# Optimization experiments

Hardware: AMD Instinct MI355X
Metric: run time of the kernel (lower is better)

## Reference

```python
import jax, jax.numpy as jnp
import numpy as np

B, S, D_IN, D_OUT = 8, 2048, 4096, 4096
RANK, N_ADAPTERS = 16, 8


def setup_inputs() -> dict:
    key = jax.random.key(0)
    k = jax.random.split(key, 6)
    x = jax.random.normal(k[0], (B, S, D_IN), dtype=jnp.float32)
    W = jax.random.normal(k[1], (D_OUT, D_IN), dtype=jnp.float32) * 0.02
    bias = jax.random.normal(k[2], (D_OUT,), dtype=jnp.float32) * 0.02
    lora_a = jax.random.normal(k[3], (N_ADAPTERS, RANK, D_IN), dtype=jnp.float32) * 0.02
    lora_b = jax.random.normal(k[4], (N_ADAPTERS, D_OUT, RANK), dtype=jnp.float32) * 0.02
    adapter_indices = jax.random.randint(k[5], (B,), 0, N_ADAPTERS, dtype=jnp.int64)
    return {"x": x, "W": W, "bias": bias, "lora_a": lora_a,
            "lora_b": lora_b, "adapter_indices": adapter_indices}


def reference(x, W, bias, lora_a, lora_b, adapter_indices):
    # Base linear: y = x @ W.T + bias
    base = jnp.einsum('bsi,oi->bso', x, W) + bias
    # Per-batch-element adapter gather (adapter index is shared across the seq dim)
    a = lora_a[adapter_indices]            # [B, r, D_in]
    b = lora_b[adapter_indices]            # [B, D_out, r]
    inter = jnp.einsum('bsi,bri->bsr', x, a)      # x_group @ a_i.T
    lora_out = jnp.einsum('bsr,bor->bso', inter, b)  # intermediate @ b_i.T
    return base + lora_out
```

## Files before the change

### kernel.cpp

```cpp
#include <hip/hip_runtime.h>


#define S_DIM   2048
#define DIN     4096
#define DOUT    4096
#define RANK    16
#define M_DIM   16384
#define K_DIM   DIN
#define N_DIM   DOUT

typedef __attribute__((ext_vector_type(8))) short  short8;
typedef __attribute__((ext_vector_type(4))) float  floatx4;

__device__ __forceinline__ unsigned short f2bf(float f) {
  union { float f; unsigned int u; } v; v.f = f;
  return (unsigned short)((v.u + 0x7FFFu + ((v.u >> 16) & 1u)) >> 16);
}
__device__ __forceinline__ unsigned int pk2(float a, float b) {
  return (unsigned int)f2bf(a) | ((unsigned int)f2bf(b) << 16);
}

__device__ __forceinline__ int load_adapter(const int* __restrict__ p, int b) {
  bool i64 = (p[1] == 0) & (p[3] == 0) & (p[5] == 0) & (p[7] == 0);
  return i64 ? p[2 * b] : p[b];
}

__device__ __forceinline__ void async16(const unsigned short* g, unsigned short* s) {
  __builtin_amdgcn_global_load_lds(
      (const __attribute__((address_space(1))) void*)g,
      (__attribute__((address_space(3))) void*)s, 16, 0, 0);
}

__device__ __forceinline__ void pack16_pad(const float* __restrict__ src,
                                           unsigned short* dst) {
  float4 v0 = ((const float4*)src)[0], v1 = ((const float4*)src)[1],
         v2 = ((const float4*)src)[2], v3 = ((const float4*)src)[3];
  uint4 p0, p1;
  p0.x = pk2(v0.x, v0.y); p0.y = pk2(v0.z, v0.w);
  p0.z = pk2(v1.x, v1.y); p0.w = pk2(v1.z, v1.w);
  p1.x = pk2(v2.x, v2.y); p1.y = pk2(v2.z, v2.w);
  p1.z = pk2(v3.x, v3.y); p1.w = pk2(v3.z, v3.w);
  ((uint4*)dst)[0] = p0;
  ((uint4*)dst)[1] = p1;
  uint4 z = make_uint4(0u, 0u, 0u, 0u);
  ((uint4*)dst)[2] = z;
  ((uint4*)dst)[3] = z;
}

__global__ __launch_bounds__(256) void conv_w(const float* __restrict__ w,
                                              unsigned short* __restrict__ wbf) {
  size_t base = ((size_t)blockIdx.x * 256 + threadIdx.x) * 8;
  const float4* src = (const float4*)(w + base);
  float4 f0 = src[0], f1 = src[1];
  uint4 p;
  p.x = pk2(f0.x, f0.y); p.y = pk2(f0.z, f0.w);
  p.z = pk2(f1.x, f1.y); p.w = pk2(f1.z, f1.w);
  *(uint4*)(wbf + base) = p;
}

__global__ __launch_bounds__(256) void inter_conv_x(
    const float* __restrict__ x,
    const float* __restrict__ lora_a,
    const int* __restrict__ adapters,
    unsigned short* __restrict__ xbf,
    float* __restrict__ inter) {
  __shared__ floatx4 red[4][64];
  const int tid = threadIdx.x, wave = tid >> 6, lane = tid & 63;
  const int fr = lane & 15, fq = lane >> 4;
  const int row0 = blockIdx.x * 16;
  const int adapter = load_adapter(adapters, row0 >> 11);

  const float* xp = x + (size_t)(row0 + fr) * DIN;
  unsigned short* xq = xbf + (size_t)(row0 + fr) * DIN;
  const float* ap = lora_a + ((size_t)adapter * RANK + fr) * DIN;

  floatx4 acc = {};
  const int kbeg = wave * 1024, kend = kbeg + 1024;
  for (int k0 = kbeg; k0 < kend; k0 += 32) {
    const int k = k0 + fq * 8;
    float4 a0 = *(const float4*)(xp + k);
    float4 a1 = *(const float4*)(xp + k + 4);
    uint4 apk;
    apk.x = pk2(a0.x, a0.y); apk.y = pk2(a0.z, a0.w);
    apk.z = pk2(a1.x, a1.y); apk.w = pk2(a1.z, a1.w);
    *(uint4*)(xq + k) = apk;
    float4 b0 = *(const float4*)(ap + k);
    float4 b1 = *(const float4*)(ap + k + 4);
    uint4 bpk;
    bpk.x = pk2(b0.x, b0.y); bpk.y = pk2(b0.z, b0.w);
    bpk.z = pk2(b1.x, b1.y); bpk.w = pk2(b1.z, b1.w);
    short8 af = *(short8*)&apk;
    short8 bf_ = *(short8*)&bpk;
    acc = __builtin_amdgcn_mfma_f32_16x16x32_bf16(af, bf_, acc, 0, 0, 0);
  }
  red[wave][lane] = acc;
  __syncthreads();
  if (wave == 0) {
    floatx4 s = red[0][lane] + red[1][lane] + red[2][lane] + red[3][lane];
#pragma unroll
    for (int j = 0; j < 4; ++j)
      inter[(size_t)(row0 + fq * 4 + j) * RANK + fr] = s[j];
  }
}

__global__ __launch_bounds__(256, 2) void gemm_lora(
    const unsigned short* __restrict__ A,
    const unsigned short* __restrict__ Bw,
    const float* __restrict__ bias,
    const float* __restrict__ inter,
    const float* __restrict__ lora_b,
    const int* __restrict__ adapters,
    float* __restrict__ out) {
  __shared__ unsigned short As[128 * 32];
  __shared__ unsigned short Bs[128 * 32];
  const int tid = threadIdx.x;
  const int wave = tid >> 6, lane = tid & 63;
  const int wm = wave >> 1, wn = wave & 1;
  const int row0 = blockIdx.y * 128, col0 = blockIdx.x * 128;

  const int lrow = lane >> 2, lcol = (lane & 3) * 8;
  const unsigned short* ag = A  + (size_t)(row0 + wave * 32 + lrow) * K_DIM + lcol;
  const unsigned short* bg = Bw + (size_t)(col0 + wave * 32 + lrow) * K_DIM + lcol;
  unsigned short* asd = As + wave * 1024;
  unsigned short* bsd = Bs + wave * 1024;

  const int fr = lane & 15, fq = lane >> 4;
  const unsigned short* afp = As + ((wm * 64 + fr) * 32 + fq * 8);
  const unsigned short* bfp = Bs + ((wn * 64 + fr) * 32 + fq * 8);

  floatx4 acc[4][4] = {};

  for (int k0 = 0; k0 < K_DIM; k0 += 32) {
    __syncthreads();
    async16(ag + k0, asd);
    async16(ag + k0 + (size_t)16 * K_DIM, asd + 512);
    async16(bg + k0, bsd);
    async16(bg + k0 + (size_t)16 * K_DIM, bsd + 512);
    __syncthreads();
    short8 af[4], bf[4];
#pragma unroll
    for (int i = 0; i < 4; ++i) af[i] = *(const short8*)(afp + i * 512);
#pragma unroll
    for (int i = 0; i < 4; ++i) bf[i] = *(const short8*)(bfp + i * 512);
#pragma unroll
    for (int mt = 0; mt < 4; ++mt)
#pragma unroll
      for (int nt = 0; nt < 4; ++nt)
        acc[mt][nt] = __builtin_amdgcn_mfma_f32_16x16x32_bf16(
            af[mt], bf[nt], acc[mt][nt], 0, 0, 0);
  }

  const int adapter = load_adapter(adapters, row0 >> 11);
  __syncthreads();
  if (tid < 128) {
    pack16_pad(inter + (size_t)(row0 + tid) * RANK, As + tid * 32);
  } else {
    int c = tid - 128;
    pack16_pad(lora_b + ((size_t)adapter * N_DIM + (col0 + c)) * RANK, Bs + c * 32);
  }
  __syncthreads();
  {
    short8 af[4], bf[4];
#pragma unroll
    for (int i = 0; i < 4; ++i) af[i] = *(const short8*)(afp + i * 512);
#pragma unroll
    for (int i = 0; i < 4; ++i) bf[i] = *(const short8*)(bfp + i * 512);
#pragma unroll
    for (int mt = 0; mt < 4; ++mt)
#pragma unroll
      for (int nt = 0; nt < 4; ++nt)
        acc[mt][nt] = __builtin_amdgcn_mfma_f32_16x16x32_bf16(
            af[mt], bf[nt], acc[mt][nt], 0, 0, 0);
  }

#pragma unroll
  for (int nt = 0; nt < 4; ++nt) {
    int col = col0 + wn * 64 + nt * 16 + fr;
    float bv = bias[col];
#pragma unroll
    for (int mt = 0; mt < 4; ++mt) {
      int row = row0 + wm * 64 + mt * 16 + fq * 4;
      float* op = out + (size_t)row * N_DIM + col;
#pragma unroll
      for (int j = 0; j < 4; ++j)
        op[(size_t)j * N_DIM] = acc[mt][nt][j] + bv;
    }
  }
}

extern "C" void kernel_launch(void* const* d_in, const int* in_sizes, int n_in,
                              void* d_out, int out_size, void* d_ws, size_t ws_size,
                              hipStream_t stream) {
  const float* x      = (const float*)d_in[0];
  const float* W      = (const float*)d_in[1];
  const float* bias   = (const float*)d_in[2];
  const float* lora_a = (const float*)d_in[3];
  const float* lora_b = (const float*)d_in[4];
  const int*   aidx   = (const int*)d_in[5];
  float* out = (float*)d_out;

  const size_t xbf_bytes = (size_t)M_DIM * DIN * 2;
  const size_t wbf_bytes = (size_t)N_DIM * DIN * 2;
  unsigned short* xbf = (unsigned short*)d_ws;
  unsigned short* wbf = (unsigned short*)((char*)d_ws + xbf_bytes);
  float* inter = (float*)((char*)d_ws + xbf_bytes + wbf_bytes);

  conv_w<<<dim3((size_t)N_DIM * DIN / (256 * 8)), dim3(256), 0, stream>>>(W, wbf);
  inter_conv_x<<<dim3(M_DIM / 16), dim3(256), 0, stream>>>(x, lora_a, aidx, xbf, inter);
  gemm_lora<<<dim3(N_DIM / 128, M_DIM / 128), dim3(256), 0, stream>>>(
      xbf, wbf, bias, inter, lora_b, aidx, out);
}
```

Measured before the change: 1.126 ms.

## Rewrite GEMM as 256x256 tile double-buffered ping-pong kernel with swizzled LDS

```diff
diff --git a/kernel.cpp b/kernel.cpp
--- a/kernel.cpp
+++ b/kernel.cpp
@@ -1,13 +1,15 @@
 #include <hip/hip_runtime.h>
 
 
-#define S_DIM   2048
 #define DIN     4096
 #define DOUT    4096
 #define RANK    16
 #define M_DIM   16384
 #define K_DIM   DIN
 #define N_DIM   DOUT
+#define BK      64
+#define NT      (K_DIM / BK)
+#define LDS_BYTES 131072
 
 typedef __attribute__((ext_vector_type(8))) short  short8;
 typedef __attribute__((ext_vector_type(4))) float  floatx4;
@@ -25,30 +27,14 @@
   return i64 ? p[2 * b] : p[b];
 }
 
-__device__ __forceinline__ void async16(const unsigned short* g, unsigned short* s) {
+__device__ __forceinline__ void async16(const unsigned short* g, void* s) {
   __builtin_amdgcn_global_load_lds(
       (const __attribute__((address_space(1))) void*)g,
       (__attribute__((address_space(3))) void*)s, 16, 0, 0);
 }
 
-__device__ __forceinline__ void pack16_pad(const float* __restrict__ src,
-                                           unsigned short* dst) {
-  float4 v0 = ((const float4*)src)[0], v1 = ((const float4*)src)[1],
-         v2 = ((const float4*)src)[2], v3 = ((const float4*)src)[3];
-  uint4 p0, p1;
-  p0.x = pk2(v0.x, v0.y); p0.y = pk2(v0.z, v0.w);
-  p0.z = pk2(v1.x, v1.y); p0.w = pk2(v1.z, v1.w);
-  p1.x = pk2(v2.x, v2.y); p1.y = pk2(v2.z, v2.w);
-  p1.z = pk2(v3.x, v3.y); p1.w = pk2(v3.z, v3.w);
-  ((uint4*)dst)[0] = p0;
-  ((uint4*)dst)[1] = p1;
-  uint4 z = make_uint4(0u, 0u, 0u, 0u);
-  ((uint4*)dst)[2] = z;
-  ((uint4*)dst)[3] = z;
-}
-
-__global__ __launch_bounds__(256) void conv_w(const float* __restrict__ w,
-                                              unsigned short* __restrict__ wbf) {
+__global__ __launch_bounds__(256) void conv_stream(const float* __restrict__ w,
+                                                   unsigned short* __restrict__ wbf) {
   size_t base = ((size_t)blockIdx.x * 256 + threadIdx.x) * 8;
   const float4* src = (const float4*)(w + base);
   float4 f0 = src[0], f1 = src[1];
@@ -58,40 +44,30 @@
   *(uint4*)(wbf + base) = p;
 }
 
-__global__ __launch_bounds__(256) void inter_conv_x(
-    const float* __restrict__ x,
+__global__ __launch_bounds__(256) void inter16(
+    const unsigned short* __restrict__ xbf,
     const float* __restrict__ lora_a,
     const int* __restrict__ adapters,
-    unsigned short* __restrict__ xbf,
     float* __restrict__ inter) {
   __shared__ floatx4 red[4][64];
   const int tid = threadIdx.x, wave = tid >> 6, lane = tid & 63;
   const int fr = lane & 15, fq = lane >> 4;
   const int row0 = blockIdx.x * 16;
   const int adapter = load_adapter(adapters, row0 >> 11);
-
-  const float* xp = x + (size_t)(row0 + fr) * DIN;
-  unsigned short* xq = xbf + (size_t)(row0 + fr) * DIN;
+  const unsigned short* xp = xbf + (size_t)(row0 + fr) * DIN;
   const float* ap = lora_a + ((size_t)adapter * RANK + fr) * DIN;
-
   floatx4 acc = {};
-  const int kbeg = wave * 1024, kend = kbeg + 1024;
-  for (int k0 = kbeg; k0 < kend; k0 += 32) {
+  const int kbeg = blockIdx.y * 2048 + wave * 512;
+#pragma unroll 2
+  for (int k0 = kbeg; k0 < kbeg + 512; k0 += 32) {
     const int k = k0 + fq * 8;
-    float4 a0 = *(const float4*)(xp + k);
-    float4 a1 = *(const float4*)(xp + k + 4);
-    uint4 apk;
-    apk.x = pk2(a0.x, a0.y); apk.y = pk2(a0.z, a0.w);
-    apk.z = pk2(a1.x, a1.y); apk.w = pk2(a1.z, a1.w);
-    *(uint4*)(xq + k) = apk;
+    short8 xf = *(const short8*)(xp + k);
     float4 b0 = *(const float4*)(ap + k);
     float4 b1 = *(const float4*)(ap + k + 4);
     uint4 bpk;
     bpk.x = pk2(b0.x, b0.y); bpk.y = pk2(b0.z, b0.w);
     bpk.z = pk2(b1.x, b1.y); bpk.w = pk2(b1.z, b1.w);
-    short8 af = *(short8*)&apk;
-    short8 bf_ = *(short8*)&bpk;
-    acc = __builtin_amdgcn_mfma_f32_16x16x32_bf16(af, bf_, acc, 0, 0, 0);
+    acc = __builtin_amdgcn_mfma_f32_16x16x32_bf16(xf, *(short8*)&bpk, acc, 0, 0, 0);
   }
   red[wave][lane] = acc;
   __syncthreads();
@@ -99,11 +75,23 @@
     floatx4 s = red[0][lane] + red[1][lane] + red[2][lane] + red[3][lane];
 #pragma unroll
     for (int j = 0; j < 4; ++j)
-      inter[(size_t)(row0 + fq * 4 + j) * RANK + fr] = s[j];
-  }
-}
-
-__global__ __launch_bounds__(256, 2) void gemm_lora(
+      atomicAdd(&inter[(size_t)(row0 + fq * 4 + j) * RANK + fr], s[j]);
+  }
+}
+
+#define SYNC_ENTER() do {                                   \
+    __builtin_amdgcn_sched_barrier(0);                      \
+    __builtin_amdgcn_s_barrier();                           \
+    asm volatile("s_waitcnt lgkmcnt(0)" ::: "memory");      \
+    __builtin_amdgcn_sched_barrier(0);                      \
+    __builtin_amdgcn_s_setprio(1); } while (0)
+#define SYNC_EXIT() do {                                    \
+    __builtin_amdgcn_s_setprio(0);                          \
+    __builtin_amdgcn_sched_barrier(0);                      \
+    __builtin_amdgcn_s_barrier();                           \
+    __builtin_amdgcn_sched_barrier(0); } while (0)
+
+__global__ __launch_bounds__(512, 2) void gemm256(
     const unsigned short* __restrict__ A,
     const unsigned short* __restrict__ Bw,
     const float* __restrict__ bias,
@@ -111,75 +99,170 @@
     const float* __restrict__ lora_b,
     const int* __restrict__ adapters,
     float* __restrict__ out) {
-  __shared__ unsigned short As[128 * 32];
-  __shared__ unsigned short Bs[128 * 32];
-  const int tid = threadIdx.x;
-  const int wave = tid >> 6, lane = tid & 63;
-  const int wm = wave >> 1, wn = wave & 1;
-  const int row0 = blockIdx.y * 128, col0 = blockIdx.x * 128;
-
-  const int lrow = lane >> 2, lcol = (lane & 3) * 8;
-  const unsigned short* ag = A  + (size_t)(row0 + wave * 32 + lrow) * K_DIM + lcol;
-  const unsigned short* bg = Bw + (size_t)(col0 + wave * 32 + lrow) * K_DIM + lcol;
-  unsigned short* asd = As + wave * 1024;
-  unsigned short* bsd = Bs + wave * 1024;
+  extern __shared__ char lds[];
+  const int tid  = threadIdx.x;
+  const int lane = tid & 63, wave = tid >> 6;
+  const int wm = wave >> 2, wn = wave & 3;
+
+  const int wg   = ((int)blockIdx.x & 7) * 128 + ((int)blockIdx.x >> 3);
+  const int row0 = (wg >> 4) * 256;
+  const int col0 = (wg & 15) * 256;
+
+  const int sg = (lane & 7) ^ (lane >> 3);
+  const int sr = wave * 16 + (lane >> 3);
+  const unsigned short* pA0 = A  + (size_t)(row0 + sr) * K_DIM + sg * 8;
+  const unsigned short* pB0 = Bw + (size_t)(col0 + sr) * K_DIM + sg * 8;
+  char* const dA0 = lds + wave * 2048;
+
+#define STG_A(h, kt, buf) do {                                            \
+    const unsigned short* _p = pA0 + (size_t)(h) * 128 * K_DIM + (kt) * BK; \
+    char* _d = dA0 + (buf) * 65536 + (h) * 16384;                         \
+    async16(_p, _d);                                                      \
+    async16(_p + (size_t)8 * K_DIM, _d + 1024); } while (0)
+#define STG_B(h, kt, buf) do {                                            \
+    const unsigned short* _p = pB0 + (size_t)(h) * 128 * K_DIM + (kt) * BK; \
+    char* _d = dA0 + 32768 + (buf) * 65536 + (h) * 16384;                 \
+    async16(_p, _d);                                                      \
+    async16(_p + (size_t)8 * K_DIM, _d + 1024); } while (0)
 
   const int fr = lane & 15, fq = lane >> 4;
-  const unsigned short* afp = As + ((wm * 64 + fr) * 32 + fq * 8);
-  const unsigned short* bfp = Bs + ((wn * 64 + fr) * 32 + fq * 8);
-
-  floatx4 acc[4][4] = {};
-
-  for (int k0 = 0; k0 < K_DIM; k0 += 32) {
-    __syncthreads();
-    async16(ag + k0, asd);
-    async16(ag + k0 + (size_t)16 * K_DIM, asd + 512);
-    async16(bg + k0, bsd);
-    async16(bg + k0 + (size_t)16 * K_DIM, bsd + 512);
-    __syncthreads();
-    short8 af[4], bf[4];
-#pragma unroll
-    for (int i = 0; i < 4; ++i) af[i] = *(const short8*)(afp + i * 512);
-#pragma unroll
-    for (int i = 0; i < 4; ++i) bf[i] = *(const short8*)(bfp + i * 512);
+  const int swz = (fr & 7) << 4;
+  const int kb0 = (fq * 16) ^ swz;
+  const int kb1 = (64 + fq * 16) ^ swz;
+  const int ar = wm * 64 + fr;
+  const int br = wn * 32 + fr;
+
+  floatx4 acc[8][4] = {};
+  short8 a[4][2], bl[2][2], bh[2][2];
+
+  STG_A(0, 0, 0); STG_B(0, 0, 0); STG_B(1, 0, 0); STG_A(1, 0, 0);
+  STG_A(0, 1, 1); STG_B(0, 1, 1); STG_B(1, 1, 1);
+  asm volatile("s_waitcnt vmcnt(6)" ::: "memory");
+  __builtin_amdgcn_sched_barrier(0);
+  __builtin_amdgcn_s_barrier();
+
+  for (int t = 0; t < NT; ++t) {
+    const int buf = t & 1, nbuf = buf ^ 1;
+    const char* ab = lds + buf * 65536;
+    const char* bb = ab + 32768;
+#pragma unroll
+    for (int mt = 0; mt < 4; ++mt) {
+      a[mt][0] = *(const short8*)(ab + (ar + mt * 16) * 128 + kb0);
+      a[mt][1] = *(const short8*)(ab + (ar + mt * 16) * 128 + kb1);
+    }
+#pragma unroll
+    for (int nt = 0; nt < 2; ++nt) {
+      bl[nt][0] = *(const short8*)(bb + (br + nt * 16) * 128 + kb0);
+      bl[nt][1] = *(const short8*)(bb + (br + nt * 16) * 128 + kb1);
+    }
+    if (t + 1 < NT) STG_A(1, t + 1, nbuf);
+    SYNC_ENTER();
 #pragma unroll
     for (int mt = 0; mt < 4; ++mt)
 #pragma unroll
-      for (int nt = 0; nt < 4; ++nt)
-        acc[mt][nt] = __builtin_amdgcn_mfma_f32_16x16x32_bf16(
-            af[mt], bf[nt], acc[mt][nt], 0, 0, 0);
-  }
-
+      for (int nt = 0; nt < 2; ++nt) {
+        acc[mt][nt] = __builtin_amdgcn_mfma_f32_16x16x32_bf16(a[mt][0], bl[nt][0], acc[mt][nt], 0, 0, 0);
+        acc[mt][nt] = __builtin_amdgcn_mfma_f32_16x16x32_bf16(a[mt][1], bl[nt][1], acc[mt][nt], 0, 0, 0);
+      }
+    SYNC_EXIT();
+#pragma unroll
+    for (int nt = 0; nt < 2; ++nt) {
+      bh[nt][0] = *(const short8*)(bb + (128 + br + nt * 16) * 128 + kb0);
+      bh[nt][1] = *(const short8*)(bb + (128 + br + nt * 16) * 128 + kb1);
+    }
+    if (t + 2 < NT) STG_A(0, t + 2, buf);
+    SYNC_ENTER();
+#pragma unroll
+    for (int mt = 0; mt < 4; ++mt)
+#pragma unroll
+      for (int nt = 0; nt < 2; ++nt) {
+        acc[mt][2 + nt] = __builtin_amdgcn_mfma_f32_16x16x32_bf16(a[mt][0], bh[nt][0], acc[mt][2 + nt], 0, 0, 0);
+        acc[mt][2 + nt] = __builtin_amdgcn_mfma_f32_16x16x32_bf16(a[mt][1], bh[nt][1], acc[mt][2 + nt], 0, 0, 0);
+      }
+    SYNC_EXIT();
+#pragma unroll
+    for (int mt = 0; mt < 4; ++mt) {
+      a[mt][0] = *(const short8*)(ab + (128 + ar + mt * 16) * 128 + kb0);
+      a[mt][1] = *(const short8*)(ab + (128 + ar + mt * 16) * 128 + kb1);
+    }
+    if (t + 2 < NT) STG_B(0, t + 2, buf);
+    SYNC_ENTER();
+#pragma unroll
+    for (int mt = 0; mt < 4; ++mt)
+#pragma unroll
+      for (int nt = 0; nt < 2; ++nt) {
+        acc[4 + mt][nt] = __builtin_amdgcn_mfma_f32_16x16x32_bf16(a[mt][0], bl[nt][0], acc[4 + mt][nt], 0, 0, 0);
+        acc[4 + mt][nt] = __builtin_amdgcn_mfma_f32_16x16x32_bf16(a[mt][1], bl[nt][1], acc[4 + mt][nt], 0, 0, 0);
+      }
+    SYNC_EXIT();
+    if (t + 2 < NT) {
+      STG_B(1, t + 2, buf);
+      asm volatile("s_waitcnt vmcnt(6)" ::: "memory");
+    } else {
+      asm volatile("s_waitcnt vmcnt(0)" ::: "memory");
+    }
+    SYNC_ENTER();
+#pragma unroll
+    for (int mt = 0; mt < 4; ++mt)
+#pragma unroll
+      for (int nt = 0; nt < 2; ++nt) {
+        acc[4 + mt][2 + nt] = __builtin_amdgcn_mfma_f32_16x16x32_bf16(a[mt][0], bh[nt][0], acc[4 + mt][2 + nt], 0, 0, 0);
+        acc[4 + mt][2 + nt] = __builtin_amdgcn_mfma_f32_16x16x32_bf16(a[mt][1], bh[nt][1], acc[4 + mt][2 + nt], 0, 0, 0);
+      }
+    SYNC_EXIT();
+  }
+
+  __syncthreads();
   const int adapter = load_adapter(adapters, row0 >> 11);
-  __syncthreads();
-  if (tid < 128) {
-    pack16_pad(inter + (size_t)(row0 + tid) * RANK, As + tid * 32);
-  } else {
-    int c = tid - 128;
-    pack16_pad(lora_b + ((size_t)adapter * N_DIM + (col0 + c)) * RANK, Bs + c * 32);
+  {
+    const int r = tid & 255;
+    const float* src = (tid < 256)
+        ? (inter + (size_t)(row0 + r) * RANK)
+        : (lora_b + ((size_t)adapter * N_DIM + (col0 + r)) * RANK);
+    char* dst = lds + ((tid < 256) ? 0 : 32768) + r * 128;
+    const float4 v0 = ((const float4*)src)[0];
+    const float4 v1 = ((const float4*)src)[1];
+    const float4 v2 = ((const float4*)src)[2];
+    const float4 v3 = ((const float4*)src)[3];
+    uint4 p0, p1;
+    p0.x = pk2(v0.x, v0.y); p0.y = pk2(v0.z, v0.w);
+    p0.z = pk2(v1.x, v1.y); p0.w = pk2(v1.z, v1.w);
+    p1.x = pk2(v2.x, v2.y); p1.y = pk2(v2.z, v2.w);
+    p1.z = pk2(v3.x, v3.y); p1.w = pk2(v3.z, v3.w);
+    const int sw = (r & 7) << 4;
+    *(uint4*)(dst + (0  ^ sw)) = p0;
+    *(uint4*)(dst + (16 ^ sw)) = p1;
+    uint4 z = make_uint4(0u, 0u, 0u, 0u);
+    *(uint4*)(dst + (32 ^ sw)) = z;
+    *(uint4*)(dst + (48 ^ sw)) = z;
   }
   __syncthreads();
   {
-    short8 af[4], bf[4];
-#pragma unroll
-    for (int i = 0; i < 4; ++i) af[i] = *(const short8*)(afp + i * 512);
-#pragma unroll
-    for (int i = 0; i < 4; ++i) bf[i] = *(const short8*)(bfp + i * 512);
-#pragma unroll
-    for (int mt = 0; mt < 4; ++mt)
+    short8 la[8], lb[4];
+#pragma unroll
+    for (int mt = 0; mt < 8; ++mt) {
+      const int rl = (mt < 4 ? wm * 64 + mt * 16 : 128 + wm * 64 + (mt - 4) * 16) + fr;
+      la[mt] = *(const short8*)(lds + rl * 128 + ((fq * 16) ^ swz));
+    }
+#pragma unroll
+    for (int nt = 0; nt < 4; ++nt) {
+      const int cl = (nt < 2 ? wn * 32 + nt * 16 : 128 + wn * 32 + (nt - 2) * 16) + fr;
+      lb[nt] = *(const short8*)(lds + 32768 + cl * 128 + ((fq * 16) ^ swz));
+    }
+#pragma unroll
+    for (int mt = 0; mt < 8; ++mt)
 #pragma unroll
       for (int nt = 0; nt < 4; ++nt)
-        acc[mt][nt] = __builtin_amdgcn_mfma_f32_16x16x32_bf16(
-            af[mt], bf[nt], acc[mt][nt], 0, 0, 0);
+        acc[mt][nt] = __builtin_amdgcn_mfma_f32_16x16x32_bf16(la[mt], lb[nt], acc[mt][nt], 0, 0, 0);
   }
 
 #pragma unroll
   for (int nt = 0; nt < 4; ++nt) {
-    int col = col0 + wn * 64 + nt * 16 + fr;
-    float bv = bias[col];
-#pragma unroll
-    for (int mt = 0; mt < 4; ++mt) {
-      int row = row0 + wm * 64 + mt * 16 + fq * 4;
+    const int col = col0 + (nt < 2 ? wn * 32 + nt * 16 : 128 + wn * 32 + (nt - 2) * 16) + fr;
+    const float bv = bias[col];
+#pragma unroll
+    for (int mt = 0; mt < 8; ++mt) {
+      const int row = row0 + (mt < 4 ? wm * 64 + mt * 16 : 128 + wm * 64 + (mt - 4) * 16) + fq * 4;
       float* op = out + (size_t)row * N_DIM + col;
 #pragma unroll
       for (int j = 0; j < 4; ++j)
@@ -205,8 +288,17 @@
   unsigned short* wbf = (unsigned short*)((char*)d_ws + xbf_bytes);
   float* inter = (float*)((char*)d_ws + xbf_bytes + wbf_bytes);
 
-  conv_w<<<dim3((size_t)N_DIM * DIN / (256 * 8)), dim3(256), 0, stream>>>(W, wbf);
-  inter_conv_x<<<dim3(M_DIM / 16), dim3(256), 0, stream>>>(x, lora_a, aidx, xbf, inter);
-  gemm_lora<<<dim3(N_DIM / 128, M_DIM / 128), dim3(256), 0, stream>>>(
+  static bool attr_set = false;
+  if (!attr_set) {
+    hipFuncSetAttribute((const void*)gemm256,
+                        hipFuncAttributeMaxDynamicSharedMemorySize, LDS_BYTES);
+    attr_set = true;
+  }
+
+  conv_stream<<<dim3((size_t)N_DIM * DIN / (256 * 8)), dim3(256), 0, stream>>>(W, wbf);
+  conv_stream<<<dim3((size_t)M_DIM * DIN / (256 * 8)), dim3(256), 0, stream>>>(x, xbf);
+  hipMemsetAsync(inter, 0, (size_t)M_DIM * RANK * sizeof(float), stream);
+  inter16<<<dim3(M_DIM / 16, 2), dim3(256), 0, stream>>>(xbf, lora_a, aidx, inter);
+  gemm256<<<dim3(1024), dim3(512), LDS_BYTES, stream>>>(
       xbf, wbf, bias, inter, lora_b, aidx, out);
 }
```

After: 975.7 us. 1.15x faster.
